# Optimization experiments

Measured on AMD Instinct MI355X. Metric: run time of the kernel, lower is better.

Reference implementation:

```python
import jax, jax.numpy as jnp
import numpy as np

H_GRID = 24
W_GRID = 24
NUM_HEADS = 3
FEAT_DIM = 192
HEAD_DIM = FEAT_DIM // NUM_HEADS  # 64
SCALE = HEAD_DIM ** -0.5
LN_EPS = 1e-5


def _positional():
    # matches get_positional_encodings with intrinsics=None; depends only on grid
    ys = jnp.linspace(-1.0, 1.0, H_GRID)
    xs = jnp.linspace(-1.0, 1.0, W_GRID)
    p3 = jnp.tile(ys, W_GRID)            # [N]
    p4 = jnp.repeat(xs, H_GRID)          # [N]
    p2 = p3 * p4
    p1 = p4 * p4
    p0 = p3 * p3
    return jnp.stack([p0, p1, p2, p3, p4, jnp.ones_like(p0)], axis=1)  # [N, 6]


def _layernorm(x, w, b):
    mu = jnp.mean(x, axis=-1, keepdims=True)
    var = jnp.mean((x - mu) ** 2, axis=-1, keepdims=True)
    return (x - mu) / jnp.sqrt(var + LN_EPS) * w + b


def _qkv_heads(x, qkv_w):
    # x: [B, N, C] -> q,k,v each [B, H, N, hd]
    B, N, _ = x.shape
    qkv = x @ qkv_w.T                                    # [B, N, 3*F]
    qkv = qkv.reshape(B, N, 3, NUM_HEADS, HEAD_DIM)
    qkv = jnp.transpose(qkv, (2, 0, 3, 1, 4))            # [3, B, H, N, hd]
    return qkv[0], qkv[1], qkv[2]


def _dual_softmax(attn):
    return jax.nn.softmax(attn, axis=-1) * jax.nn.softmax(attn, axis=-2)


def setup_inputs() -> dict:
    key = jax.random.key(0)
    ks = jax.random.split(key, 4)
    B, C = 64, 256
    in_dim, out_dim = C, 512
    dim_size = 2 * NUM_HEADS * (HEAD_DIM + 6) * (HEAD_DIM + 6)  # 29400
    return {
        "x1": jax.random.normal(ks[0], (B, C, H_GRID, W_GRID), jnp.float32),
        "x2": jax.random.normal(ks[1], (B, C, H_GRID, W_GRID), jnp.float32),
        "ln_w": jnp.ones((in_dim,), jnp.float32),
        "ln_b": jnp.zeros((in_dim,), jnp.float32),
        "qkv_w": jax.random.normal(ks[2], (3 * FEAT_DIM, in_dim), jnp.float32) * (in_dim ** -0.5),
        "proj_w": jax.random.normal(ks[3], (out_dim, dim_size), jnp.float32) * (dim_size ** -0.5),
        "proj_b": jnp.zeros((out_dim,), jnp.float32),
    }


def reference(x1, x2, ln_w, ln_b, qkv_w, proj_w, proj_b):
    B, C, h, w = x1.shape
    N = h * w
    x1t = _layernorm(x1.reshape(B, C, N).transpose(0, 2, 1), ln_w, ln_b)  # [B, N, C]
    x2t = _layernorm(x2.reshape(B, C, N).transpose(0, 2, 1), ln_w, ln_b)

    q1, k1, v1 = _qkv_heads(x1t, qkv_w)
    q2, k2, v2 = _qkv_heads(x2t, qkv_w)

    attn_1 = jnp.einsum("bhnd,bhmd->bhnm", q2, k1) * SCALE
    attn_2 = jnp.einsum("bhnd,bhmd->bhnm", q1, k2) * SCALE
    af1 = _dual_softmax(attn_1)
    af2 = _dual_softmax(attn_2)

    pos = jnp.broadcast_to(_positional(), (B, NUM_HEADS, N, 6))
    v1p = jnp.concatenate([v1, pos], axis=-1)  # [B, H, N, hd+6]
    v2p = jnp.concatenate([v2, pos], axis=-1)

    f1 = jnp.einsum("bhnd,bhnm,bhme->bhde", v1p, af1, v1p)  # [B, H, hd+6, hd+6]
    f2 = jnp.einsum("bhnd,bhnm,bhme->bhde", v2p, af2, v2p)

    feat = jnp.concatenate([f1.reshape(B, -1), f2.reshape(B, -1)], axis=-1)
    return jax.nn.relu(feat @ proj_w.T + proj_b)
```

## Files before the change

### kernel.cpp

```cpp
#include <hip/hip_runtime.h>

#define NSEQ 576
#define CDIM 256
#define HEADS 3
#define HD 64
#define FEAT 192
#define QKVF 576
#define QK_F 384
#define VP 70
#define BHN 192
#define DIMSZ 29400

typedef __attribute__((ext_vector_type(8))) _Float16 half8;
typedef __attribute__((ext_vector_type(4))) _Float16 half4;
typedef __attribute__((ext_vector_type(4))) float f32x4;

#define MFMA16(A,B,C) __builtin_amdgcn_mfma_f32_16x16x32_f16(A,B,C,0,0,0)

__device__ __forceinline__ float posval(int n, int pe){
  int yi = n % 24, xi = n / 24;
  float py = (float)yi * (2.0f/23.0f) - 1.0f;
  float px = (float)xi * (2.0f/23.0f) - 1.0f;
  switch(pe){
    case 0: return py*py;
    case 1: return px*px;
    case 2: return py*px;
    case 3: return py;
    case 4: return px;
    default: return 1.0f;
  }
}

template<int LD>
__device__ __forceinline__ half8 fragT(const _Float16 (*s)[LD], int row, int dbase){
  half4 a = *(const half4*)&s[row][dbase];
  half4 b = *(const half4*)&s[row][dbase + 16];
  return __builtin_shufflevector(a, b, 0, 1, 2, 3, 4, 5, 6, 7);
}

__device__ __forceinline__ void stage_copy64(const _Float16* __restrict__ src, int rstr,
                                             _Float16 (*d)[72], int t){
  #pragma unroll
  for (int k2 = 0; k2 < 2; ++k2){
    int idx = t + 256 * k2;
    int row = idx >> 3, c = (idx & 7) << 3;
    half8 v = *(const half8*)(src + (size_t)row * rstr + c);
    *(half4*)&d[row][c]     = (half4){v[0], v[1], v[2], v[3]};
    *(half4*)&d[row][c + 4] = (half4){v[4], v[5], v[6], v[7]};
  }
}

__device__ __forceinline__ int rotIdx(int row, int c16){
  return row * 64 + ((((c16) + row) & 7) << 3);
}

__global__ __launch_bounds__(192) void k_ln_stats(const float* __restrict__ x1, const float* __restrict__ x2,
                                                  float* __restrict__ mu, float* __restrict__ rstd){
  int idx = blockIdx.x;
  int i2 = idx / 192;
  int rem = idx % 192;
  int b = rem / 3, ng = rem % 3;
  int n = ng * 192 + threadIdx.x;
  const float* x = i2 ? x2 : x1;
  const float* xb = x + (size_t)b * CDIM * NSEQ + n;
  float s = 0.f, sq = 0.f;
  for (int c = 0; c < CDIM; ++c){
    float v = xb[(size_t)c * NSEQ];
    s += v; sq += v * v;
  }
  float m = s * (1.0f/256.0f);
  float var = sq * (1.0f/256.0f) - m * m;
  int o = (i2 * 64 + b) * NSEQ + n;
  mu[o] = m;
  rstd[o] = rsqrtf(var + 1e-5f);
}

__global__ __launch_bounds__(256) void k_w_repack(const float* __restrict__ qkvw,
                                                  _Float16* __restrict__ wrh, _Float16* __restrict__ wrl){
  int idx = blockIdx.x * 256 + threadIdx.x;
  if (idx >= 18432) return;
  int fi = idx & 63;
  int r = idx >> 6;
  int hi = r & 3; r >>= 2;
  int kc = r & 1; r >>= 1;
  int cb = r & 3; r >>= 2;
  int ft = r;
  int f = ft * 64 + fi;
  int cbase = cb * 64 + kc * 32 + hi * 4;
  const float* src = qkvw + (size_t)f * CDIM + cbase;
  float4 a = *(const float4*)src;
  float4 b = *(const float4*)(src + 16);
  float vv[8] = {a.x, a.y, a.z, a.w, b.x, b.y, b.z, b.w};
  half8 h, l;
  #pragma unroll
  for (int j = 0; j < 8; ++j){
    _Float16 hh = (_Float16)vv[j];
    h[j] = hh;
    l[j] = (_Float16)(vv[j] - (float)hh);
  }
  *(half8*)(wrh + (size_t)idx * 8) = h;
  *(half8*)(wrl + (size_t)idx * 8) = l;
}

__global__ __launch_bounds__(256) void k_qkv_gemm_mfma(const float* __restrict__ x1, const float* __restrict__ x2,
                                                       const float* __restrict__ mu, const float* __restrict__ rstd,
                                                       const float* __restrict__ lnw, const float* __restrict__ lnb,
                                                       const _Float16* __restrict__ wrh, const _Float16* __restrict__ wrl,
                                                       _Float16* __restrict__ qh, _Float16* __restrict__ ql,
                                                       _Float16* __restrict__ vpTh, _Float16* __restrict__ vpTl){
  int wg = (blockIdx.x & 7) * 1296 + (blockIdx.x >> 3);
  int ft = wg % 9;
  int mt = wg / 9;
  int ibn = mt * 64;
  int i2 = ibn / (64 * NSEQ);
  int bn = ibn % (64 * NSEQ);
  int b  = bn / NSEQ;
  int n0 = bn % NSEQ;
  const float* x = i2 ? x2 : x1;
  const float* xb = x + (size_t)b * CDIM * NSEQ + n0;
  __shared__ __align__(16) _Float16 Xh[64][68];
  __shared__ __align__(16) _Float16 Xl[64][68];
  __shared__ float smu[64], srstd[64], slnw[256], slnb[256];
  int t = threadIdx.x;
  int w = t >> 6, lane = t & 63, tx = lane & 15, hi = lane >> 4;
  if (t < 64){ smu[t] = mu[ibn + t]; srstd[t] = rstd[ibn + t]; }
  slnw[t] = lnw[t]; slnb[t] = lnb[t];

  f32x4 acc[4];
  #pragma unroll
  for (int s = 0; s < 4; ++s) acc[s] = (f32x4){0.f, 0.f, 0.f, 0.f};

  int nA = t & 63, cg = t >> 6;
  int lchunk = hi * 64 + w * 16 + tx;
  for (int c0 = 0; c0 < CDIM; c0 += 64){
    int cb = c0 >> 6;
    __syncthreads();
    float mun = smu[nA], rsn = srstd[nA];
    #pragma unroll
    for (int rr = 0; rr < 16; ++rr){
      int c = cg * 16 + rr;
      float v = xb[(size_t)(c0 + c) * NSEQ + nA];
      float xv = (v - mun) * rsn * slnw[c0 + c] + slnb[c0 + c];
      _Float16 hh = (_Float16)xv;
      Xh[nA][c] = hh;
      Xl[nA][c] = (_Float16)(xv - (float)hh);
    }
    __syncthreads();
    #pragma unroll
    for (int kc = 0; kc < 2; ++kc){
      size_t wo = ((size_t)((ft * 4 + cb) * 2 + kc) * 256 + lchunk) * 8;
      half8 wh = *(const half8*)(wrh + wo);
      half8 wl = *(const half8*)(wrl + wo);
      #pragma unroll
      for (int s = 0; s < 4; ++s){
        half8 xh = fragT<68>(Xh, s * 16 + tx, kc * 32 + hi * 4);
        half8 xl = fragT<68>(Xl, s * 16 + tx, kc * 32 + hi * 4);
        acc[s] = MFMA16(xh, wh, acc[s]);
        acc[s] = MFMA16(xl, wh, acc[s]);
        acc[s] = MFMA16(xh, wl, acc[s]);
      }
    }
  }
  if (ft < 6){
    #pragma unroll
    for (int s = 0; s < 4; ++s)
      #pragma unroll
      for (int rr = 0; rr < 4; ++rr){
        float v = acc[s][rr];
        _Float16 hh = (_Float16)v;
        size_t o = (size_t)(ibn + s * 16 + hi * 4 + rr) * QK_F + ft * 64 + w * 16 + tx;
        qh[o] = hh;
        ql[o] = (_Float16)(v - (float)hh);
      }
  } else {
    __syncthreads();
    #pragma unroll
    for (int s = 0; s < 4; ++s)
      #pragma unroll
      for (int rr = 0; rr < 4; ++rr){
        float v = acc[s][rr];
        _Float16 hh = (_Float16)v;
        Xh[s * 16 + hi * 4 + rr][w * 16 + tx] = hh;
        Xl[s * 16 + hi * 4 + rr][w * 16 + tx] = (_Float16)(v - (float)hh);
      }
    __syncthreads();
    int mbg = i2 * 192 + b * 3 + (ft - 6);
    #pragma unroll
    for (int it = 0; it < 16; ++it){
      int d = (t >> 6) + it * 4;
      int n2 = t & 63;
      size_t o = ((size_t)mbg * 80 + d) * NSEQ + n0 + n2;
      vpTh[o] = Xh[n2][d];
      vpTl[o] = Xl[n2][d];
    }
  }
}

__global__ __launch_bounds__(256) void k_pos_fill(_Float16* __restrict__ vpTh, _Float16* __restrict__ vpTl){
  int idx = blockIdx.x * 256 + threadIdx.x;
  if (idx >= 384 * 16 * NSEQ) return;
  int n = idx % NSEQ;
  int r = idx / NSEQ;
  int row = 64 + (r & 15);
  int mb = r >> 4;
  float v = 0.f;
  int pe = row - 64;
  if (pe < 6) v = posval(n, pe);
  _Float16 hh = (_Float16)v;
  size_t o = ((size_t)mb * 80 + row) * NSEQ + n;
  vpTh[o] = hh;
  vpTl[o] = (_Float16)(v - (float)hh);
}

__global__ __launch_bounds__(256) void k_attn_stats_mfma(const _Float16* __restrict__ qh, const _Float16* __restrict__ ql,
                                                         float* __restrict__ rs, float* __restrict__ cs_part){
  int wg = (blockIdx.x & 7) * 432 + (blockIdx.x >> 3);
  int map = wg / (BHN * 9);
  int r   = wg % (BHN * 9);
  int bh = r / 9, nt = r % 9;
  int b = bh / 3, h = bh % 3;
  int qi = 1 - map, ki = map;
  int mb = map * BHN + bh;
  const _Float16* qbh = qh + (size_t)((qi * 64 + b) * NSEQ) * QK_F + h * HD;
  const _Float16* qbl = ql + (size_t)((qi * 64 + b) * NSEQ) * QK_F + h * HD;
  const _Float16* kbh = qh + (size_t)((ki * 64 + b) * NSEQ) * QK_F + FEAT + h * HD;
  const _Float16* kbl = ql + (size_t)((ki * 64 + b) * NSEQ) * QK_F + FEAT + h * HD;
  int n0 = nt * 64;
  __shared__ __align__(16) _Float16 Kh[2][64 * 64];
  __shared__ __align__(16) _Float16 Kl[2][64 * 64];
  __shared__ float rsLds[4][64];
  int t = threadIdx.x;
  int w = t >> 6, lane = t & 63, tx = lane & 15, hi = lane >> 4;

  for (int idx = t; idx < 2048; idx += 256){
    int tile = idx >> 10;
    int hl   = (idx >> 9) & 1;
    int rc   = idx & 511;
    int row = rc >> 3, c16 = rc & 7;
    const _Float16* src = tile ? (hl ? qbl : qbh) : (hl ? kbl : kbh);
    int srow = tile ? (n0 + row) : row;
    _Float16* dst = (hl ? &Kl[tile][0] : &Kh[tile][0]);
    *(half8*)(dst + rotIdx(row, c16)) = *(const half8*)(src + (size_t)srow * QK_F + c16 * 8);
  }
  __syncthreads();
  half8 qAh[4][2], qAl[4][2];
  #pragma unroll
  for (int s = 0; s < 4; ++s)
    #pragma unroll
    for (int kc = 0; kc < 2; ++kc){
      qAh[s][kc] = *(half8*)(&Kh[1][0] + rotIdx(s * 16 + tx, kc * 4 + hi));
      qAl[s][kc] = *(half8*)(&Kl[1][0] + rotIdx(s * 16 + tx, kc * 4 + hi));
    }
  __syncthreads();

  auto stageK = [&](int mt2, int bufi){
    int m0 = mt2 * 64;
    for (int idx = t; idx < 1024; idx += 256){
      int a = idx >> 9, rc = idx & 511, row = rc >> 3, c16 = rc & 7;
      const _Float16* src = a ? kbl : kbh;
      _Float16* dst = a ? &Kl[bufi][0] : &Kh[bufi][0];
      *(half8*)(dst + rotIdx(row, c16)) = *(const half8*)(src + (size_t)(m0 + row) * QK_F + c16 * 8);
    }
  };

  float rsum[4][4] = {};
  for (int mt = 0; mt < 9; ++mt){
    int cur = mt & 1;
    int m0 = mt * 64;
    if (mt < 8) stageK(mt + 1, cur ^ 1);
    f32x4 acc[4];
    #pragma unroll
    for (int s = 0; s < 4; ++s) acc[s] = (f32x4){0.f, 0.f, 0.f, 0.f};
    #pragma unroll
    for (int kc = 0; kc < 2; ++kc){
      half8 kb8 = *(half8*)(&Kh[cur][0] + rotIdx(w * 16 + tx, kc * 4 + hi));
      half8 kl8 = *(half8*)(&Kl[cur][0] + rotIdx(w * 16 + tx, kc * 4 + hi));
      #pragma unroll
      for (int s = 0; s < 4; ++s){
        acc[s] = MFMA16(qAh[s][kc], kb8, acc[s]);
        acc[s] = MFMA16(qAl[s][kc], kb8, acc[s]);
        acc[s] = MFMA16(qAh[s][kc], kl8, acc[s]);
      }
    }
    float csum = 0.f;
    #pragma unroll
    for (int s = 0; s < 4; ++s)
      #pragma unroll
      for (int rr = 0; rr < 4; ++rr){
        float e = __expf(acc[s][rr] * 0.125f);
        rsum[s][rr] += e;
        csum += e;
      }
    csum += __shfl_xor(csum, 16);
    csum += __shfl_xor(csum, 32);
    if (lane < 16)
      cs_part[((size_t)mb * 9 + nt) * NSEQ + m0 + w * 16 + tx] = csum;
    __syncthreads();
  }
  #pragma unroll
  for (int s = 0; s < 4; ++s)
    #pragma unroll
    for (int rr = 0; rr < 4; ++rr){
      float v = rsum[s][rr];
      v += __shfl_xor(v, 1);
      v += __shfl_xor(v, 2);
      v += __shfl_xor(v, 4);
      v += __shfl_xor(v, 8);
      if (tx == 0) rsLds[w][s * 16 + hi * 4 + rr] = v;
    }
  __syncthreads();
  if (t < 64)
    rs[(size_t)mb * NSEQ + n0 + t] = rsLds[0][t] + rsLds[1][t] + rsLds[2][t] + rsLds[3][t];
}

__global__ __launch_bounds__(256) void k_cs_reduce(const float* __restrict__ cs_part, float* __restrict__ cs){
  int tid = blockIdx.x * 256 + threadIdx.x;
  if (tid >= 2 * BHN * NSEQ) return;
  int mb = tid / NSEQ, m = tid % NSEQ;
  float s = 0.f;
  #pragma unroll
  for (int p = 0; p < 9; ++p)
    s += cs_part[((size_t)mb * 9 + p) * NSEQ + m];
  cs[tid] = s;
}

__global__ __launch_bounds__(256) void k_apply_mfma(const _Float16* __restrict__ qh, const _Float16* __restrict__ ql,
                                                    const _Float16* __restrict__ vpTh, const _Float16* __restrict__ vpTl,
                                                    const float* __restrict__ rs, const float* __restrict__ cs,
                                                    _Float16* __restrict__ tTh, _Float16* __restrict__ tTl, int map){
  int wg = (blockIdx.x & 7) * 216 + (blockIdx.x >> 3);
  int bh = wg / 9, nt = wg % 9;
  int b = bh / 3, h = bh % 3;
  int qi = 1 - map, ki = map;
  int mb = map * BHN + bh;
  const _Float16* qbh = qh + (size_t)((qi * 64 + b) * NSEQ) * QK_F + h * HD;
  const _Float16* qbl = ql + (size_t)((qi * 64 + b) * NSEQ) * QK_F + h * HD;
  const _Float16* kbh = qh + (size_t)((ki * 64 + b) * NSEQ) * QK_F + FEAT + h * HD;
  const _Float16* kbl = ql + (size_t)((ki * 64 + b) * NSEQ) * QK_F + FEAT + h * HD;
  const _Float16* vTh = vpTh + (size_t)mb * 80 * NSEQ;
  const _Float16* vTl = vpTl + (size_t)mb * 80 * NSEQ;
  int n0 = nt * 64;
  __shared__ __align__(16) _Float16 Ash[64][72];
  __shared__ __align__(16) _Float16 Asl[64][72];
  __shared__ __align__(16) _Float16 Vth[80][72];
  __shared__ __align__(16) _Float16 Vtl[80][72];
  __shared__ float cinv[64];
  int t = threadIdx.x;
  int w = t >> 6, lane = t & 63, tx = lane & 15, hi = lane >> 4;

  stage_copy64(qbh + (size_t)n0 * QK_F, QK_F, Ash, t);
  stage_copy64(qbl + (size_t)n0 * QK_F, QK_F, Asl, t);
  __syncthreads();
  half8 qB0h = fragT<72>(Ash, w * 16 + tx, 0 + hi * 4);
  half8 qB1h = fragT<72>(Ash, w * 16 + tx, 32 + hi * 4);
  half8 qB0l = fragT<72>(Asl, w * 16 + tx, 0 + hi * 4);
  half8 qB1l = fragT<72>(Asl, w * 16 + tx, 32 + hi * 4);
  float rinv = 1.0f / rs[(size_t)mb * NSEQ + n0 + w * 16 + tx];

  half8 kPh[2], kPl[2];
  auto loadK = [&](int mt2){
    int m0 = mt2 * 64;
    #pragma unroll
    for (int k2 = 0; k2 < 2; ++k2){
      int idx = t + 256 * k2;
      int row = idx >> 3, c = (idx & 7) << 3;
      kPh[k2] = *(const half8*)(kbh + (size_t)(m0 + row) * QK_F + c);
      kPl[k2] = *(const half8*)(kbl + (size_t)(m0 + row) * QK_F + c);
    }
  };
  loadK(0);

  f32x4 tacc[5];
  #pragma unroll
  for (int et = 0; et < 5; ++et) tacc[et] = (f32x4){0.f, 0.f, 0.f, 0.f};

  for (int mt = 0; mt < 9; ++mt){
    int m0 = mt * 64;
    __syncthreads();
    #pragma unroll
    for (int k2 = 0; k2 < 2; ++k2){
      int idx = t + 256 * k2;
      int row = idx >> 3, c = (idx & 7) << 3;
      half8 vh = kPh[k2], vl = kPl[k2];
      *(half4*)&Ash[row][c]     = (half4){vh[0], vh[1], vh[2], vh[3]};
      *(half4*)&Ash[row][c + 4] = (half4){vh[4], vh[5], vh[6], vh[7]};
      *(half4*)&Asl[row][c]     = (half4){vl[0], vl[1], vl[2], vl[3]};
      *(half4*)&Asl[row][c + 4] = (half4){vl[4], vl[5], vl[6], vl[7]};
    }
    #pragma unroll
    for (int k2 = 0; k2 < 3; ++k2){
      int idx = t + 256 * k2;
      if (idx < 640){
        int row = idx >> 3, c = (idx & 7) << 3;
        half8 v1 = *(const half8*)(vTh + (size_t)row * NSEQ + m0 + c);
        *(half4*)&Vth[row][c]     = (half4){v1[0], v1[1], v1[2], v1[3]};
        *(half4*)&Vth[row][c + 4] = (half4){v1[4], v1[5], v1[6], v1[7]};
        half8 v2 = *(const half8*)(vTl + (size_t)row * NSEQ + m0 + c);
        *(half4*)&Vtl[row][c]     = (half4){v2[0], v2[1], v2[2], v2[3]};
        *(half4*)&Vtl[row][c + 4] = (half4){v2[4], v2[5], v2[6], v2[7]};
      }
    }
    if (t < 64) cinv[t] = 1.0f / cs[(size_t)mb * NSEQ + m0 + t];
    __syncthreads();
    if (mt < 8) loadK(mt + 1);

    f32x4 acc[4];
    #pragma unroll
    for (int s = 0; s < 4; ++s) acc[s] = (f32x4){0.f, 0.f, 0.f, 0.f};
    #pragma unroll
    for (int s = 0; s < 4; ++s){
      half8 kh0 = fragT<72>(Ash, s * 16 + tx, 0 + hi * 4);
      half8 kl0 = fragT<72>(Asl, s * 16 + tx, 0 + hi * 4);
      half8 kh1 = fragT<72>(Ash, s * 16 + tx, 32 + hi * 4);
      half8 kl1 = fragT<72>(Asl, s * 16 + tx, 32 + hi * 4);
      acc[s] = MFMA16(kh0, qB0h, acc[s]);
      acc[s] = MFMA16(kl0, qB0h, acc[s]);
      acc[s] = MFMA16(kh0, qB0l, acc[s]);
      acc[s] = MFMA16(kh1, qB1h, acc[s]);
      acc[s] = MFMA16(kl1, qB1h, acc[s]);
      acc[s] = MFMA16(kh1, qB1l, acc[s]);
    }
    half8 bph[2], bpl[2];
    #pragma unroll
    for (int s = 0; s < 4; ++s){
      #pragma unroll
      for (int rr = 0; rr < 4; ++rr){
        float af = __expf(acc[s][rr] * 0.25f) * rinv * cinv[s * 16 + hi * 4 + rr];
        _Float16 hh = (_Float16)af;
        bph[s >> 1][(s & 1) * 4 + rr] = hh;
        bpl[s >> 1][(s & 1) * 4 + rr] = (_Float16)(af - (float)hh);
      }
    }
    #pragma unroll
    for (int et = 0; et < 5; ++et)
      #pragma unroll
      for (int mc = 0; mc < 2; ++mc){
        half8 vhf = fragT<72>(Vth, et * 16 + tx, mc * 32 + hi * 4);
        half8 vlf = fragT<72>(Vtl, et * 16 + tx, mc * 32 + hi * 4);
        tacc[et] = MFMA16(vhf, bph[mc], tacc[et]);
        tacc[et] = MFMA16(vhf, bpl[mc], tacc[et]);
        tacc[et] = MFMA16(vlf, bph[mc], tacc[et]);
      }
  }
  #pragma unroll
  for (int et = 0; et < 5; ++et)
    #pragma unroll
    for (int rr = 0; rr < 4; ++rr){
      int e = et * 16 + hi * 4 + rr;
      float v = tacc[et][rr];
      _Float16 hh = (_Float16)v;
      size_t o = ((size_t)bh * 80 + e) * NSEQ + n0 + w * 16 + tx;
      tTh[o] = hh;
      tTl[o] = (_Float16)(v - (float)hh);
    }
}

__global__ __launch_bounds__(256) void k_f_gemm_mfma(const _Float16* __restrict__ vpTh, const _Float16* __restrict__ vpTl,
                                                     const _Float16* __restrict__ tTh, const _Float16* __restrict__ tTl,
                                                     float* __restrict__ featT3, int map){
  int wg = blockIdx.x;
  int mbL = wg / 3, part = wg % 3;
  int b = mbL / 3, h = mbL % 3;
  __shared__ __align__(16) _Float16 Ah[80][40], Al[80][40], Bh[80][40], Bl[80][40];
  int t = threadIdx.x;
  int w4 = t >> 6, lane = t & 63, tx = lane & 15, hi = lane >> 4;
  const _Float16* Abh = vpTh + (size_t)(map * BHN + mbL) * 80 * NSEQ;
  const _Float16* Abl = vpTl + (size_t)(map * BHN + mbL) * 80 * NSEQ;
  const _Float16* Bbh = tTh + (size_t)mbL * 80 * NSEQ;
  const _Float16* Bbl = tTl + (size_t)mbL * 80 * NSEQ;
  f32x4 acc[7];
  #pragma unroll
  for (int j = 0; j < 7; ++j) acc[j] = (f32x4){0.f, 0.f, 0.f, 0.f};

  for (int kc = part * 6; kc < part * 6 + 6; ++kc){
    int c0 = kc * 32;
    __syncthreads();
    #pragma unroll
    for (int k2 = 0; k2 < 2; ++k2){
      int idx = t + 256 * k2;
      if (idx < 320){
        int row = idx >> 2, cc = (idx & 3) << 3;
        *(half8*)&Ah[row][cc] = *(const half8*)(Abh + (size_t)row * NSEQ + c0 + cc);
        *(half8*)&Al[row][cc] = *(const half8*)(Abl + (size_t)row * NSEQ + c0 + cc);
        *(half8*)&Bh[row][cc] = *(const half8*)(Bbh + (size_t)row * NSEQ + c0 + cc);
        *(half8*)&Bl[row][cc] = *(const half8*)(Bbl + (size_t)row * NSEQ + c0 + cc);
      }
    }
    __syncthreads();
    #pragma unroll
    for (int j = 0; j < 7; ++j){
      int ti = w4 + 4 * j;
      if (ti < 25){
        int db = ti / 5, eb = ti % 5;
        half8 ah = *(const half8*)&Ah[db * 16 + tx][hi * 8];
        half8 al = *(const half8*)&Al[db * 16 + tx][hi * 8];
        half8 bh = *(const half8*)&Bh[eb * 16 + tx][hi * 8];
        half8 bl = *(const half8*)&Bl[eb * 16 + tx][hi * 8];
        acc[j] = MFMA16(ah, bh, acc[j]);
        acc[j] = MFMA16(al, bh, acc[j]);
        acc[j] = MFMA16(ah, bl, acc[j]);
      }
    }
  }
  #pragma unroll
  for (int j = 0; j < 7; ++j){
    int ti = w4 + 4 * j;
    if (ti < 25){
      int db = ti / 5, eb = ti % 5;
      #pragma unroll
      for (int rr = 0; rr < 4; ++rr){
        int d = db * 16 + hi * 4 + rr, e = eb * 16 + tx;
        if (d < VP && e < VP)
          featT3[(size_t)part * 1881600 + (size_t)(map * 14700 + h * 4900 + d * VP + e) * 64 + b] = acc[j][rr];
      }
    }
  }
}

__global__ __launch_bounds__(256) void k_feat_reduce(const float* __restrict__ featT3, float* __restrict__ featT){
  int gid = blockIdx.x * 256 + threadIdx.x;
  if (gid >= DIMSZ * 64) return;
  featT[gid] = featT3[gid] + featT3[1881600 + gid] + featT3[2 * 1881600 + gid];
}

__global__ __launch_bounds__(256) void k_proj_gemm(const float* __restrict__ featT, const float* __restrict__ pw,
                                                   float* __restrict__ p){
  int ot = blockIdx.x & 7;
  int s  = blockIdx.x >> 3;
  int o0 = ot * 64;
  int kbase = s * 300;
  __shared__ __align__(16) float As[20][72];
  __shared__ __align__(16) float Bs[20][72];
  int t = threadIdx.x, tx = t & 15, ty = t >> 4;
  float acc[4][4] = {};
  for (int kt = 0; kt < 15; ++kt){
    int k0 = kbase + kt * 20;
    __syncthreads();
    #pragma unroll
    for (int r = 0; r < 5; ++r){
      int idx = t + 256 * r;
      int bb = idx & 63, kk = idx >> 6;
      As[kk][bb] = featT[(size_t)(k0 + kk) * 64 + bb];
      int ko = idx % 20, oo = idx / 20;
      Bs[ko][oo] = pw[(size_t)(o0 + oo) * DIMSZ + k0 + ko];
    }
    __syncthreads();
    #pragma unroll
    for (int k = 0; k < 20; ++k){
      float4 a4 = *(const float4*)&As[k][ty * 4];
      float4 b4 = *(const float4*)&Bs[k][tx * 4];
      float aa[4] = {a4.x, a4.y, a4.z, a4.w};
      float bb[4] = {b4.x, b4.y, b4.z, b4.w};
      #pragma unroll
      for (int i = 0; i < 4; ++i)
        #pragma unroll
        for (int j = 0; j < 4; ++j)
          acc[i][j] += aa[i] * bb[j];
    }
  }
  int slice = s * 8 + ot;
  #pragma unroll
  for (int i = 0; i < 4; ++i){
    float4 st = make_float4(acc[i][0], acc[i][1], acc[i][2], acc[i][3]);
    *(float4*)&p[(size_t)slice * 4096 + (ty * 4 + i) * 64 + tx * 4] = st;
  }
}

__global__ __launch_bounds__(256) void k_finalize(const float* __restrict__ p, const float* __restrict__ pb,
                                                  float* __restrict__ out){
  int gid = blockIdx.x * 256 + threadIdx.x;
  int o = gid & 511, b = gid >> 9;
  int ot = o >> 6, lo = o & 63;
  float s = pb[o];
  for (int s2 = 0; s2 < 98; ++s2)
    s += p[(size_t)(s2 * 8 + ot) * 4096 + b * 64 + lo];
  out[gid] = fmaxf(s, 0.0f);
}

extern "C" void kernel_launch(void* const* d_in, const int* in_sizes, int n_in,
                              void* d_out, int out_size, void* d_ws, size_t ws_size,
                              hipStream_t stream) {
  const float* x1   = (const float*)d_in[0];
  const float* x2   = (const float*)d_in[1];
  const float* lnw  = (const float*)d_in[2];
  const float* lnb  = (const float*)d_in[3];
  const float* qkvw = (const float*)d_in[4];
  const float* pw   = (const float*)d_in[5];
  const float* pb   = (const float*)d_in[6];
  float* out = (float*)d_out;

  float* w = (float*)d_ws;
  float*     mu      = w;
  float*     rstd    = w + 73728;
  _Float16*  qh      = (_Float16*)(w + 147456);
  _Float16*  ql      = (_Float16*)(w + 14303232);
  _Float16*  vpTh    = (_Float16*)(w + 28459008);
  _Float16*  vpTl    = (_Float16*)(w + 37306368);
  _Float16*  tTh     = (_Float16*)(w + 46153728);
  _Float16*  tTl     = (_Float16*)(w + 50577408);
  float*     cs_part = w + 55001088;
  float*     featT   = w + 55001088;
  float*     rs      = w + 56991744;
  float*     cs      = w + 57212928;
  float*     featT3  = w + 57434112;
  float*     p       = w + 57434112;
  _Float16*  wrh     = (_Float16*)(w + 60645376);
  _Float16*  wrl     = (_Float16*)(w + 60719104);

  k_ln_stats<<<384, 192, 0, stream>>>(x1, x2, mu, rstd);
  k_w_repack<<<72, 256, 0, stream>>>(qkvw, wrh, wrl);
  k_qkv_gemm_mfma<<<10368, 256, 0, stream>>>(x1, x2, mu, rstd, lnw, lnb, wrh, wrl, qh, ql, vpTh, vpTl);
  k_pos_fill<<<13824, 256, 0, stream>>>(vpTh, vpTl);
  k_attn_stats_mfma<<<3456, 256, 0, stream>>>(qh, ql, rs, cs_part);
  k_cs_reduce<<<864, 256, 0, stream>>>(cs_part, cs);
  for (int map = 0; map < 2; ++map){
    k_apply_mfma<<<1728, 256, 0, stream>>>(qh, ql, vpTh, vpTl, rs, cs, tTh, tTl, map);
    k_f_gemm_mfma<<<576, 256, 0, stream>>>(vpTh, vpTl, tTh, tTl, featT3, map);
  }
  k_feat_reduce<<<7350, 256, 0, stream>>>(featT3, featT);
  k_proj_gemm<<<784, 256, 0, stream>>>(featT, pw, p);
  k_finalize<<<128, 256, 0, stream>>>(p, pb, out);
}
```

Baseline: 691.1 us.

## Give each wave a private K slice, drop per-tile block barriers in attn stats

The attention statistics kernel now splits the 576 key rows into four contiguous 144-row ranges, one per wave. Each wave stages its own 16-row K chunks through a private LDS region with register prefetch, so the per-iteration __syncthreads is gone and shared memory per block is halved. Launch bounds ask for 4 blocks per CU to raise occupancy. The risk is that intra-wave LDS write-then-read ordering relies on wave-level execution with no explicit barrier, and the register pressure from the prefetch buffers must fit the occupancy target.

```diff
diff --git a/kernel.cpp b/kernel.cpp
--- a/kernel.cpp
+++ b/kernel.cpp
@@ -212,8 +212,8 @@
   vpTl[o] = (_Float16)(v - (float)hh);
 }
 
-__global__ __launch_bounds__(256) void k_attn_stats_mfma(const _Float16* __restrict__ qh, const _Float16* __restrict__ ql,
-                                                         float* __restrict__ rs, float* __restrict__ cs_part){
+__global__ __launch_bounds__(256, 4) void k_attn_stats_mfma(const _Float16* __restrict__ qh, const _Float16* __restrict__ ql,
+                                                            float* __restrict__ rs, float* __restrict__ cs_part){
   int wg = (blockIdx.x & 7) * 432 + (blockIdx.x >> 3);
   int map = wg / (BHN * 9);
   int r   = wg % (BHN * 9);
@@ -226,21 +226,17 @@
   const _Float16* kbh = qh + (size_t)((ki * 64 + b) * NSEQ) * QK_F + FEAT + h * HD;
   const _Float16* kbl = ql + (size_t)((ki * 64 + b) * NSEQ) * QK_F + FEAT + h * HD;
   int n0 = nt * 64;
-  __shared__ __align__(16) _Float16 Kh[2][64 * 64];
-  __shared__ __align__(16) _Float16 Kl[2][64 * 64];
+  __shared__ __align__(16) _Float16 Sh[4096];
+  __shared__ __align__(16) _Float16 Sl[4096];
   __shared__ float rsLds[4][64];
   int t = threadIdx.x;
   int w = t >> 6, lane = t & 63, tx = lane & 15, hi = lane >> 4;
 
-  for (int idx = t; idx < 2048; idx += 256){
-    int tile = idx >> 10;
-    int hl   = (idx >> 9) & 1;
-    int rc   = idx & 511;
-    int row = rc >> 3, c16 = rc & 7;
-    const _Float16* src = tile ? (hl ? qbl : qbh) : (hl ? kbl : kbh);
-    int srow = tile ? (n0 + row) : row;
-    _Float16* dst = (hl ? &Kl[tile][0] : &Kh[tile][0]);
-    *(half8*)(dst + rotIdx(row, c16)) = *(const half8*)(src + (size_t)srow * QK_F + c16 * 8);
+  for (int idx = t; idx < 1024; idx += 256){
+    int a = idx >> 9, rc = idx & 511, row = rc >> 3, c16 = rc & 7;
+    const _Float16* src = a ? qbl : qbh;
+    _Float16* dst = a ? Sl : Sh;
+    *(half8*)(dst + rotIdx(row, c16)) = *(const half8*)(src + (size_t)(n0 + row) * QK_F + c16 * 8);
   }
   __syncthreads();
   half8 qAh[4][2], qAl[4][2];
@@ -248,33 +244,44 @@
   for (int s = 0; s < 4; ++s)
     #pragma unroll
     for (int kc = 0; kc < 2; ++kc){
-      qAh[s][kc] = *(half8*)(&Kh[1][0] + rotIdx(s * 16 + tx, kc * 4 + hi));
-      qAl[s][kc] = *(half8*)(&Kl[1][0] + rotIdx(s * 16 + tx, kc * 4 + hi));
+      qAh[s][kc] = *(half8*)(Sh + rotIdx(s * 16 + tx, kc * 4 + hi));
+      qAl[s][kc] = *(half8*)(Sl + rotIdx(s * 16 + tx, kc * 4 + hi));
     }
   __syncthreads();
 
-  auto stageK = [&](int mt2, int bufi){
-    int m0 = mt2 * 64;
-    for (int idx = t; idx < 1024; idx += 256){
-      int a = idx >> 9, rc = idx & 511, row = rc >> 3, c16 = rc & 7;
-      const _Float16* src = a ? kbl : kbh;
-      _Float16* dst = a ? &Kl[bufi][0] : &Kh[bufi][0];
-      *(half8*)(dst + rotIdx(row, c16)) = *(const half8*)(src + (size_t)(m0 + row) * QK_F + c16 * 8);
+  _Float16* kh = Sh + w * 1024;
+  _Float16* kl = Sl + w * 1024;
+  int mw0 = w * 144;
+  half8 kPh[2], kPl[2];
+  auto loadK = [&](int i){
+    int m0r = mw0 + i * 16;
+    #pragma unroll
+    for (int p = 0; p < 2; ++p){
+      int ch = p * 64 + lane;
+      int row = ch >> 3, c16 = ch & 7;
+      kPh[p] = *(const half8*)(kbh + (size_t)(m0r + row) * QK_F + c16 * 8);
+      kPl[p] = *(const half8*)(kbl + (size_t)(m0r + row) * QK_F + c16 * 8);
     }
   };
+  loadK(0);
 
   float rsum[4][4] = {};
-  for (int mt = 0; mt < 9; ++mt){
-    int cur = mt & 1;
-    int m0 = mt * 64;
-    if (mt < 8) stageK(mt + 1, cur ^ 1);
+  for (int i = 0; i < 9; ++i){
+    #pragma unroll
+    for (int p = 0; p < 2; ++p){
+      int ch = p * 64 + lane;
+      int row = ch >> 3, c16 = ch & 7;
+      *(half8*)(kh + rotIdx(row, c16)) = kPh[p];
+      *(half8*)(kl + rotIdx(row, c16)) = kPl[p];
+    }
+    if (i < 8) loadK(i + 1);
     f32x4 acc[4];
     #pragma unroll
     for (int s = 0; s < 4; ++s) acc[s] = (f32x4){0.f, 0.f, 0.f, 0.f};
     #pragma unroll
     for (int kc = 0; kc < 2; ++kc){
-      half8 kb8 = *(half8*)(&Kh[cur][0] + rotIdx(w * 16 + tx, kc * 4 + hi));
-      half8 kl8 = *(half8*)(&Kl[cur][0] + rotIdx(w * 16 + tx, kc * 4 + hi));
+      half8 kb8 = *(half8*)(kh + rotIdx(tx, kc * 4 + hi));
+      half8 kl8 = *(half8*)(kl + rotIdx(tx, kc * 4 + hi));
       #pragma unroll
       for (int s = 0; s < 4; ++s){
         acc[s] = MFMA16(qAh[s][kc], kb8, acc[s]);
@@ -294,8 +301,7 @@
     csum += __shfl_xor(csum, 16);
     csum += __shfl_xor(csum, 32);
     if (lane < 16)
-      cs_part[((size_t)mb * 9 + nt) * NSEQ + m0 + w * 16 + tx] = csum;
-    __syncthreads();
+      cs_part[((size_t)mb * 9 + nt) * NSEQ + mw0 + i * 16 + tx] = csum;
   }
   #pragma unroll
   for (int s = 0; s < 4; ++s)
```

Measured after the change: 814.7 us. +17.9%, slower.
